# Kernel optimization log

Measured on AMD Instinct MI355X. Metric: run time of the kernel, lower is better.

Reference implementation:

```python
import jax, jax.numpy as jnp
import numpy as np

BIG = 5000.0  # knockout sentinel from the original code
LOSS_WEIGHTS = jnp.array([1.0, 1.0, 1.0, 1.0, 1.0])  # [prob, x, y, a, b]


def _build_targets(preds, targets):
    """Greedy confidence-sorted matching for one batch element.
    preds: [N, 5] (prob, x, y, a, b); targets: [M, 5].
    Returns built targets [N, 5] aligned with the original pred order.
    """
    conf = preds[:, 0]
    order = jnp.argsort(-conf)          # descending confidence
    sp = preds[order]                   # [N, 5] sorted preds
    valid = targets[:, 0] == 1.0        # replaces the torch boolean filter
    n_targs = valid.sum()
    n_pos = (conf > 0.5).sum()
    M = targets.shape[0]

    def step(used, inp):
        i, p = inp
        x, y = p[1], p[2]
        # knocked-out targets sit at (BIG, BIG), matching the in-place write
        tx = jnp.where(used, BIG, targets[:, 1])
        ty = jnp.where(used, BIG, targets[:, 2])
        d2 = (tx - x) ** 2 + (ty - y) ** 2
        d2 = jnp.where(valid, d2, jnp.inf)  # invalid targets were filtered out
        min_idx = jnp.argmin(d2)
        row_nearest = jnp.stack([
            targets[min_idx, 0], tx[min_idx], ty[min_idx],
            targets[min_idx, 3], targets[min_idx, 4],
        ])
        # first valid, not-yet-chosen target (notchosen = x < 5000)
        first_idx = jnp.argmax(valid & (~used))
        row_first = targets[first_idx]
        # false positive: keep pred's continuous vars, prob target = 0
        row_fp = p.at[0].set(0.0)

        case_match = (i < n_pos) & (i < n_targs)   # greedy nearest match + knockout
        case_first = (~case_match) & (i < n_targs)  # n_pos <= i < n_targs
        row = jnp.where(case_match, row_nearest,
                        jnp.where(case_first, row_first, row_fp))
        used = jnp.where(case_match, used.at[min_idx].set(True), used)
        return used, row

    used0 = jnp.zeros(M, dtype=bool)
    _, built = jax.lax.scan(step, used0, (jnp.arange(sp.shape[0]), sp))
    # undo the confidence sort: built_targs[argsort(sort_conf)]
    return built[jnp.argsort(order)]


def setup_inputs() -> dict:
    key = jax.random.key(0)
    k1, k2, k3 = jax.random.split(key, 3)
    B, N, M = 256, 2048, 512
    preds = jax.random.uniform(k1, (B, N, 5), dtype=jnp.float32)  # prob in (0,1) for BCE
    tprob = (jax.random.uniform(k2, (B, M, 1)) > 0.5).astype(jnp.float32)  # ~half valid
    tvals = jax.random.uniform(k3, (B, M, 4), dtype=jnp.float32)
    targets = jnp.concatenate([tprob, tvals], axis=-1)
    return {"preds": preds, "targets": targets}


def reference(preds, targets):
    # built targets are constants w.r.t. autograd (requires_grad=False in torch)
    built = jax.lax.stop_gradient(jax.vmap(_build_targets)(preds, targets))
    p = preds[..., 0]
    t = built[..., 0]
    # BCE with torch's log clamp at -100
    logp = jnp.clip(jnp.log(p), -100.0)
    log1mp = jnp.clip(jnp.log1p(-p), -100.0)
    lossprob = -jnp.mean(t * logp + (1.0 - t) * log1mp) * LOSS_WEIGHTS[0]
    mse = lambda c: jnp.mean((preds[..., c] - built[..., c]) ** 2)
    lossx = mse(1) * LOSS_WEIGHTS[1]
    lossy = mse(2) * LOSS_WEIGHTS[2]
    lossa = mse(3) * LOSS_WEIGHTS[3]
    lossb = mse(4) * LOSS_WEIGHTS[4]
    # dict {'lossx','lossy','lossa','lossb','lossprob'} packed as a 5-vector
    return jnp.stack([lossx, lossy, lossa, lossb, lossprob])
```

## Files before the change

### kernel.cpp

```cpp
#include <hip/hip_runtime.h>
#include <stdint.h>

#define NPRED 2048
#define MT    512
#define BLK   256
#define NCAND 512

template<int C>
__device__ __forceinline__ uint32_t dppminu(uint32_t v) {
  uint32_t o = (uint32_t)__builtin_amdgcn_update_dpp((int)v, (int)v, C, 0xF, 0xF, false);
  return v < o ? v : o;
}
__device__ __forceinline__ uint32_t wave_min_u32_l63(uint32_t v) {
  v = dppminu<0x111>(v); v = dppminu<0x112>(v); v = dppminu<0x114>(v);
  v = dppminu<0x118>(v); v = dppminu<0x142>(v); v = dppminu<0x143>(v);
  return (uint32_t)__builtin_amdgcn_readlane((int)v, 63);
}
__device__ __forceinline__ uint32_t rowmin16(uint32_t v) {
  v = dppminu<0x111>(v); v = dppminu<0x112>(v);
  v = dppminu<0x114>(v); v = dppminu<0x118>(v);
  return v;
}

__global__ __launch_bounds__(BLK, 1) void loss_kernel(const float* __restrict__ preds,
                                                      const float* __restrict__ targets,
                                                      double* __restrict__ acc) {
  const int b = blockIdx.x;
  const float* __restrict__ P = preds   + (size_t)b * NPRED * 5;
  const float* __restrict__ T = targets + (size_t)b * MT * 5;

  __shared__ uint64_t keys[NPRED];
  __shared__ uint64_t cand[NCAND];
  __shared__ float txy[MT * 2];
  __shared__ float tab[MT * 2];
  __shared__ float spx[520], spy[520], spa[520], spb[520];
  __shared__ uint16_t plds[512];
  __shared__ int hist[256];
  __shared__ uint32_t validw[16];
  __shared__ int s_npos, s_nt, s_B, s_ncand, s_first;
  __shared__ uint64_t s_thr;
  __shared__ double red[5][BLK];

  const int tid = threadIdx.x;
  if (tid == 0) { s_npos = 0; s_nt = 0; s_B = 0; s_ncand = 0; s_first = 0; s_thr = 0ull; }
  hist[tid] = 0;
  if (tid < 16) validw[tid] = 0;
  for (int i = tid; i < 520; i += BLK) { spx[i] = 0.f; spy[i] = 0.f; spa[i] = 0.f; spb[i] = 0.f; }
  __syncthreads();

  int cpos = 0;
  for (int i = tid; i < NPRED; i += BLK) {
    float c = P[i * 5 + 0];
    cpos += (c > 0.5f) ? 1 : 0;
    uint32_t cb = __float_as_uint(c);
    keys[i] = ((uint64_t)(~cb) << 32) | (uint32_t)i;
    if (cb >= 0x3F000000u && cb < 0x3F800000u)
      atomicAdd(&hist[(cb >> 15) & 0xFF], 1);
  }
  atomicAdd(&s_npos, cpos);

  int ct = 0;
  for (int m = tid; m < MT; m += BLK) {
    float tp = T[m * 5 + 0];
    bool v = (tp == 1.0f);
    if (v) { ct++; atomicOr(&validw[m >> 5], 1u << (m & 31)); }
    txy[2 * m]     = T[m * 5 + 1];
    txy[2 * m + 1] = T[m * 5 + 2];
    tab[2 * m]     = T[m * 5 + 3];
    tab[2 * m + 1] = T[m * 5 + 4];
  }
  atomicAdd(&s_nt, ct);
  __syncthreads();
  const int n_pos = s_npos;
  const int n_targs = s_nt;

  if (tid < 64) {
    const int lane = tid;
    int4 h4 = *reinterpret_cast<const int4*>(&hist[lane * 4]);
    int t = h4.x + h4.y + h4.z + h4.w;
    int S = t;
#pragma unroll
    for (int off = 1; off < 64; off <<= 1) {
      int o = __shfl_down(S, off);
      if (lane + off < 64) S += o;
    }
    int Snext = S - t;
    int s3 = h4.w + Snext;
    int s2 = h4.z + s3;
    int s1 = h4.y + s2;
    int s0 = h4.x + s1;
    int localB = -1;
    if      (s3 >= n_targs) localB = lane * 4 + 3;
    else if (s2 >= n_targs) localB = lane * 4 + 2;
    else if (s1 >= n_targs) localB = lane * 4 + 1;
    else if (s0 >= n_targs) localB = lane * 4 + 0;
    uint64_t q = __ballot(localB >= 0);
    if (q) {
      int hl = 63 - __clzll((long long)q);
      int B = __builtin_amdgcn_readlane(localB, hl);
      if (lane == 0) s_B = B;
    }
  }
  __syncthreads();
  const int B = s_B;

  for (int i = tid; i < NPRED; i += BLK) {
    uint64_t k = keys[i];
    uint32_t cb = ~(uint32_t)(k >> 32);
    if (cb >= 0x3F000000u && cb < 0x3F800000u && (int)((cb >> 15) & 0xFF) >= B) {
      int slot = atomicAdd(&s_ncand, 1);
      if (slot < NCAND) cand[slot] = k;
    }
  }
  __syncthreads();
  const int ncand = min(s_ncand, NCAND);

  {
    uint64_t ka = (tid < ncand) ? cand[tid] : ~0ull;
    uint64_t kb = (tid + BLK < ncand) ? cand[tid + BLK] : ~0ull;
    int ra = 0, rb = 0;
    for (int j = 0; j < ncand; ++j) {
      uint64_t kj = cand[j];
      ra += (kj < ka) ? 1 : 0;
      rb += (kj < kb) ? 1 : 0;
    }
    if (tid < ncand && ra < n_targs) {
      int idx = (int)(ka & 0xFFFFFFFFu);
      spx[ra] = P[idx * 5 + 1]; spy[ra] = P[idx * 5 + 2];
      spa[ra] = P[idx * 5 + 3]; spb[ra] = P[idx * 5 + 4];
    }
    if (tid < ncand && ra == n_targs - 1) s_thr = ka;
    if (tid + BLK < ncand && rb < n_targs) {
      int idx = (int)(kb & 0xFFFFFFFFu);
      spx[rb] = P[idx * 5 + 1]; spy[rb] = P[idx * 5 + 2];
      spa[rb] = P[idx * 5 + 3]; spb[rb] = P[idx * 5 + 4];
    }
    if (tid + BLK < ncand && rb == n_targs - 1) s_thr = kb;
  }
  __syncthreads();
  const uint64_t thr = s_thr;
  const int K = min(n_pos, n_targs);

  float accp = 0.f;

  if (tid < 64) {
    const int lane = tid;
    const int s = lane & 15;
    const int g = lane >> 4;
    const uint32_t sbase = (uint32_t)(s << 5);

    float txr[32], tyr[32];
#pragma unroll
    for (int j = 0; j < 32; ++j) {
      txr[j] = txy[2 * (s * 32 + j)];
      tyr[j] = txy[2 * (s * 32 + j) + 1];
    }
    uint32_t una = ~validw[s];

    int i = 0;
    float x1 = spx[g], y1 = spy[g];
    float x2 = spx[4 + g], y2 = spy[4 + g];
    while (i + 8 <= K) {
      uint32_t kk1 = 0xFFFFFFFFu, kk2 = 0xFFFFFFFFu;
#pragma unroll
      for (int j = 0; j < 32; ++j) {
        uint32_t pois = 0u - ((una >> j) & 1u);
        {
          float dx = __fsub_rn(txr[j], x1);
          float dy = __fsub_rn(tyr[j], y1);
          float d2 = __fadd_rn(__fmul_rn(dx, dx), __fmul_rn(dy, dy));
          uint32_t key = ((__float_as_uint(d2) & 0xFFFFFE00u) | (sbase + (uint32_t)j)) | pois;
          kk1 = kk1 < key ? kk1 : key;
        }
        {
          float dx = __fsub_rn(txr[j], x2);
          float dy = __fsub_rn(tyr[j], y2);
          float d2 = __fadd_rn(__fmul_rn(dx, dx), __fmul_rn(dy, dy));
          uint32_t key = ((__float_as_uint(d2) & 0xFFFFFE00u) | (sbase + (uint32_t)j)) | pois;
          kk2 = kk2 < key ? kk2 : key;
        }
      }
      kk1 = rowmin16(kk1);
      kk2 = rowmin16(kk2);
      int m0 = __builtin_amdgcn_readlane((int)kk1, 15) & 0x1FF;
      int m1 = __builtin_amdgcn_readlane((int)kk1, 31) & 0x1FF;
      int m2 = __builtin_amdgcn_readlane((int)kk1, 47) & 0x1FF;
      int m3 = __builtin_amdgcn_readlane((int)kk1, 63) & 0x1FF;
      int m4 = __builtin_amdgcn_readlane((int)kk2, 15) & 0x1FF;
      int m5 = __builtin_amdgcn_readlane((int)kk2, 31) & 0x1FF;
      int m6 = __builtin_amdgcn_readlane((int)kk2, 47) & 0x1FF;
      int m7 = __builtin_amdgcn_readlane((int)kk2, 63) & 0x1FF;

      bool c1 = (m1==m0);
      bool c2 = (m2==m0)|(m2==m1);
      bool c3 = (m3==m0)|(m3==m1)|(m3==m2);
      bool c4 = (m4==m0)|(m4==m1)|(m4==m2)|(m4==m3);
      bool c5 = (m5==m0)|(m5==m1)|(m5==m2)|(m5==m3)|(m5==m4);
      bool c6 = (m6==m0)|(m6==m1)|(m6==m2)|(m6==m3)|(m6==m4)|(m6==m5);
      bool c7 = (m7==m0)|(m7==m1)|(m7==m2)|(m7==m3)|(m7==m4)|(m7==m5)|(m7==m6);
      int p = c1 ? 1 : c2 ? 2 : c3 ? 3 : c4 ? 4 : c5 ? 5 : c6 ? 6 : c7 ? 7 : 8;

      int m1e = (p > 1) ? m1 : 0x3FF;
      int m2e = (p > 2) ? m2 : 0x3FF;
      int m3e = (p > 3) ? m3 : 0x3FF;
      int m4e = (p > 4) ? m4 : 0x3FF;
      int m5e = (p > 5) ? m5 : 0x3FF;
      int m6e = (p > 6) ? m6 : 0x3FF;
      int m7e = (p > 7) ? m7 : 0x3FF;

      una |= ((uint32_t)(m0  >> 5) == (uint32_t)s) ? (1u << (m0  & 31)) : 0u;
      una |= ((uint32_t)(m1e >> 5) == (uint32_t)s) ? (1u << (m1e & 31)) : 0u;
      una |= ((uint32_t)(m2e >> 5) == (uint32_t)s) ? (1u << (m2e & 31)) : 0u;
      una |= ((uint32_t)(m3e >> 5) == (uint32_t)s) ? (1u << (m3e & 31)) : 0u;
      una |= ((uint32_t)(m4e >> 5) == (uint32_t)s) ? (1u << (m4e & 31)) : 0u;
      una |= ((uint32_t)(m5e >> 5) == (uint32_t)s) ? (1u << (m5e & 31)) : 0u;
      una |= ((uint32_t)(m6e >> 5) == (uint32_t)s) ? (1u << (m6e & 31)) : 0u;
      una |= ((uint32_t)(m7e >> 5) == (uint32_t)s) ? (1u << (m7e & 31)) : 0u;

      if (lane == 0) {
        plds[i]     = (uint16_t)m0;
        plds[i + 1] = (uint16_t)m1e;
        plds[i + 2] = (uint16_t)m2e;
        plds[i + 3] = (uint16_t)m3e;
        plds[i + 4] = (uint16_t)m4e;
        plds[i + 5] = (uint16_t)m5e;
        plds[i + 6] = (uint16_t)m6e;
        plds[i + 7] = (uint16_t)m7e;
      }
      i += p;
      x1 = spx[i + g];     y1 = spy[i + g];
      x2 = spx[i + 4 + g]; y2 = spy[i + 4 + g];
    }
    while (i < K) {
      float xs = spx[i], ys = spy[i];
      uint32_t kk = 0xFFFFFFFFu;
#pragma unroll
      for (int j = 0; j < 32; ++j) {
        float dx = __fsub_rn(txr[j], xs);
        float dy = __fsub_rn(tyr[j], ys);
        float d2 = __fadd_rn(__fmul_rn(dx, dx), __fmul_rn(dy, dy));
        uint32_t pois = 0u - ((una >> j) & 1u);
        uint32_t key = ((__float_as_uint(d2) & 0xFFFFFE00u) | (sbase + (uint32_t)j)) | pois;
        kk = kk < key ? kk : key;
      }
      kk = rowmin16(kk);
      uint32_t m = (uint32_t)__builtin_amdgcn_readlane((int)kk, 15) & 0x1FFu;
      una |= ((m >> 5) == (uint32_t)s) ? (1u << (m & 31u)) : 0u;
      if (lane == 0) plds[i] = (uint16_t)m;
      ++i;
    }
    uint32_t av = ~una;
    uint32_t fi = av ? (sbase + (uint32_t)__ffs(av) - 1u) : 0xFFFFFFFFu;
    fi = wave_min_u32_l63(fi);
    if (lane == 0) s_first = (fi < MT) ? (int)fi : 0;
  } else {
    for (int i = tid - 64; i < NPRED; i += (BLK - 64)) {
      uint64_t k = keys[i];
      float p = __uint_as_float(~(uint32_t)(k >> 32));
      accp += (k <= thr) ? -fmaxf(logf(p), -100.0f)
                         : -fmaxf(log1pf(-p), -100.0f);
    }
  }
  __syncthreads();

  float ax = 0.f, ay = 0.f, aa = 0.f, ab = 0.f;
  for (int r = tid; r < K; r += BLK) {
    int m = plds[r];
    float dx = __fsub_rn(spx[r], txy[2 * m]);
    float dy = __fsub_rn(spy[r], txy[2 * m + 1]);
    float da = __fsub_rn(spa[r], tab[2 * m]);
    float db = __fsub_rn(spb[r], tab[2 * m + 1]);
    ax += __fmul_rn(dx, dx);
    ay += __fmul_rn(dy, dy);
    aa += __fmul_rn(da, da);
    ab += __fmul_rn(db, db);
  }
  if (n_pos < n_targs) {
    int f = s_first;
    float fx = txy[2 * f], fy = txy[2 * f + 1];
    float fa = tab[2 * f], fb = tab[2 * f + 1];
    for (int i2 = n_pos + tid; i2 < n_targs; i2 += BLK) {
      float dx = __fsub_rn(spx[i2], fx);
      float dy = __fsub_rn(spy[i2], fy);
      float da = __fsub_rn(spa[i2], fa);
      float db = __fsub_rn(spb[i2], fb);
      ax += __fmul_rn(dx, dx);
      ay += __fmul_rn(dy, dy);
      aa += __fmul_rn(da, da);
      ab += __fmul_rn(db, db);
    }
  }

  red[0][tid] = (double)ax;
  red[1][tid] = (double)ay;
  red[2][tid] = (double)aa;
  red[3][tid] = (double)ab;
  red[4][tid] = (double)accp;
  __syncthreads();
  for (int st = BLK / 2; st > 0; st >>= 1) {
    if (tid < st) {
#pragma unroll
      for (int c = 0; c < 5; ++c) red[c][tid] += red[c][tid + st];
    }
    __syncthreads();
  }
  if (tid == 0) {
#pragma unroll
    for (int c = 0; c < 5; ++c) atomicAdd(&acc[c], red[c][0]);
  }
}

__global__ void finalize_kernel(const double* __restrict__ acc,
                                float* __restrict__ out, double inv) {
  int c = threadIdx.x;
  if (c < 5) out[c] = (float)(acc[c] * inv);
}

extern "C" void kernel_launch(void* const* d_in, const int* in_sizes, int n_in,
                              void* d_out, int out_size, void* d_ws, size_t ws_size,
                              hipStream_t stream) {
  const float* preds = (const float*)d_in[0];
  const float* targets = (const float*)d_in[1];
  int B = in_sizes[0] / (NPRED * 5);

  double* acc = (double*)d_ws;
  hipMemsetAsync(acc, 0, 5 * sizeof(double), stream);
  loss_kernel<<<B, BLK, 0, stream>>>(preds, targets, acc);
  finalize_kernel<<<1, 64, 0, stream>>>(acc, (float*)d_out,
                                        1.0 / ((double)B * NPRED));
}
```

Measured before the change: 93.07 us.

## Narrow speculative matching to four preds per wave with split min chains

```diff
diff --git a/kernel.cpp b/kernel.cpp
--- a/kernel.cpp
+++ b/kernel.cpp
@@ -158,93 +158,87 @@
     uint32_t una = ~validw[s];
 
     int i = 0;
-    float x1 = spx[g], y1 = spy[g];
-    float x2 = spx[4 + g], y2 = spy[4 + g];
-    while (i + 8 <= K) {
-      uint32_t kk1 = 0xFFFFFFFFu, kk2 = 0xFFFFFFFFu;
-#pragma unroll
-      for (int j = 0; j < 32; ++j) {
-        uint32_t pois = 0u - ((una >> j) & 1u);
+    float x = spx[g], y = spy[g];
+    while (i + 4 <= K) {
+      float nx1 = spx[i + 1 + g], ny1 = spy[i + 1 + g];
+      float nx2 = spx[i + 2 + g], ny2 = spy[i + 2 + g];
+      float nx3 = spx[i + 3 + g], ny3 = spy[i + 3 + g];
+      float nx4 = spx[i + 4 + g], ny4 = spy[i + 4 + g];
+
+      uint32_t ke = 0xFFFFFFFFu, ko = 0xFFFFFFFFu;
+#pragma unroll
+      for (int j = 0; j < 32; j += 2) {
         {
-          float dx = __fsub_rn(txr[j], x1);
-          float dy = __fsub_rn(tyr[j], y1);
+          float dx = __fsub_rn(txr[j], x);
+          float dy = __fsub_rn(tyr[j], y);
           float d2 = __fadd_rn(__fmul_rn(dx, dx), __fmul_rn(dy, dy));
-          uint32_t key = ((__float_as_uint(d2) & 0xFFFFFE00u) | (sbase + (uint32_t)j)) | pois;
-          kk1 = kk1 < key ? kk1 : key;
+          uint32_t pois = (uint32_t)(((int32_t)(una << (31 - j))) >> 31);
+          uint32_t key = ((__float_as_uint(d2) | pois) & 0xFFFFFE00u) | (uint32_t)j;
+          ke = ke < key ? ke : key;
         }
         {
-          float dx = __fsub_rn(txr[j], x2);
-          float dy = __fsub_rn(tyr[j], y2);
+          float dx = __fsub_rn(txr[j + 1], x);
+          float dy = __fsub_rn(tyr[j + 1], y);
           float d2 = __fadd_rn(__fmul_rn(dx, dx), __fmul_rn(dy, dy));
-          uint32_t key = ((__float_as_uint(d2) & 0xFFFFFE00u) | (sbase + (uint32_t)j)) | pois;
-          kk2 = kk2 < key ? kk2 : key;
+          uint32_t pois = (uint32_t)(((int32_t)(una << (31 - (j + 1)))) >> 31);
+          uint32_t key = ((__float_as_uint(d2) | pois) & 0xFFFFFE00u) | (uint32_t)(j + 1);
+          ko = ko < key ? ko : key;
         }
       }
-      kk1 = rowmin16(kk1);
-      kk2 = rowmin16(kk2);
-      int m0 = __builtin_amdgcn_readlane((int)kk1, 15) & 0x1FF;
-      int m1 = __builtin_amdgcn_readlane((int)kk1, 31) & 0x1FF;
-      int m2 = __builtin_amdgcn_readlane((int)kk1, 47) & 0x1FF;
-      int m3 = __builtin_amdgcn_readlane((int)kk1, 63) & 0x1FF;
-      int m4 = __builtin_amdgcn_readlane((int)kk2, 15) & 0x1FF;
-      int m5 = __builtin_amdgcn_readlane((int)kk2, 31) & 0x1FF;
-      int m6 = __builtin_amdgcn_readlane((int)kk2, 47) & 0x1FF;
-      int m7 = __builtin_amdgcn_readlane((int)kk2, 63) & 0x1FF;
-
-      bool c1 = (m1==m0);
-      bool c2 = (m2==m0)|(m2==m1);
-      bool c3 = (m3==m0)|(m3==m1)|(m3==m2);
-      bool c4 = (m4==m0)|(m4==m1)|(m4==m2)|(m4==m3);
-      bool c5 = (m5==m0)|(m5==m1)|(m5==m2)|(m5==m3)|(m5==m4);
-      bool c6 = (m6==m0)|(m6==m1)|(m6==m2)|(m6==m3)|(m6==m4)|(m6==m5);
-      bool c7 = (m7==m0)|(m7==m1)|(m7==m2)|(m7==m3)|(m7==m4)|(m7==m5)|(m7==m6);
-      int p = c1 ? 1 : c2 ? 2 : c3 ? 3 : c4 ? 4 : c5 ? 5 : c6 ? 6 : c7 ? 7 : 8;
-
+      uint32_t kk = ke < ko ? ke : ko;
+      uint32_t kkg = rowmin16(kk + sbase);
+      int m0 = __builtin_amdgcn_readlane((int)kkg, 15) & 0x1FF;
+      int m1 = __builtin_amdgcn_readlane((int)kkg, 31) & 0x1FF;
+      int m2 = __builtin_amdgcn_readlane((int)kkg, 47) & 0x1FF;
+      int m3 = __builtin_amdgcn_readlane((int)kkg, 63) & 0x1FF;
+
+      int p = (m1 == m0) ? 1
+            : (m2 == m0 || m2 == m1) ? 2
+            : (m3 == m0 || m3 == m1 || m3 == m2) ? 3 : 4;
       int m1e = (p > 1) ? m1 : 0x3FF;
       int m2e = (p > 2) ? m2 : 0x3FF;
       int m3e = (p > 3) ? m3 : 0x3FF;
-      int m4e = (p > 4) ? m4 : 0x3FF;
-      int m5e = (p > 5) ? m5 : 0x3FF;
-      int m6e = (p > 6) ? m6 : 0x3FF;
-      int m7e = (p > 7) ? m7 : 0x3FF;
 
       una |= ((uint32_t)(m0  >> 5) == (uint32_t)s) ? (1u << (m0  & 31)) : 0u;
       una |= ((uint32_t)(m1e >> 5) == (uint32_t)s) ? (1u << (m1e & 31)) : 0u;
       una |= ((uint32_t)(m2e >> 5) == (uint32_t)s) ? (1u << (m2e & 31)) : 0u;
       una |= ((uint32_t)(m3e >> 5) == (uint32_t)s) ? (1u << (m3e & 31)) : 0u;
-      una |= ((uint32_t)(m4e >> 5) == (uint32_t)s) ? (1u << (m4e & 31)) : 0u;
-      una |= ((uint32_t)(m5e >> 5) == (uint32_t)s) ? (1u << (m5e & 31)) : 0u;
-      una |= ((uint32_t)(m6e >> 5) == (uint32_t)s) ? (1u << (m6e & 31)) : 0u;
-      una |= ((uint32_t)(m7e >> 5) == (uint32_t)s) ? (1u << (m7e & 31)) : 0u;
 
       if (lane == 0) {
         plds[i]     = (uint16_t)m0;
         plds[i + 1] = (uint16_t)m1e;
         plds[i + 2] = (uint16_t)m2e;
         plds[i + 3] = (uint16_t)m3e;
-        plds[i + 4] = (uint16_t)m4e;
-        plds[i + 5] = (uint16_t)m5e;
-        plds[i + 6] = (uint16_t)m6e;
-        plds[i + 7] = (uint16_t)m7e;
       }
       i += p;
-      x1 = spx[i + g];     y1 = spy[i + g];
-      x2 = spx[i + 4 + g]; y2 = spy[i + 4 + g];
+      x = (p == 1) ? nx1 : (p == 2) ? nx2 : (p == 3) ? nx3 : nx4;
+      y = (p == 1) ? ny1 : (p == 2) ? ny2 : (p == 3) ? ny3 : ny4;
     }
     while (i < K) {
       float xs = spx[i], ys = spy[i];
-      uint32_t kk = 0xFFFFFFFFu;
-#pragma unroll
-      for (int j = 0; j < 32; ++j) {
-        float dx = __fsub_rn(txr[j], xs);
-        float dy = __fsub_rn(tyr[j], ys);
-        float d2 = __fadd_rn(__fmul_rn(dx, dx), __fmul_rn(dy, dy));
-        uint32_t pois = 0u - ((una >> j) & 1u);
-        uint32_t key = ((__float_as_uint(d2) & 0xFFFFFE00u) | (sbase + (uint32_t)j)) | pois;
-        kk = kk < key ? kk : key;
+      uint32_t ke = 0xFFFFFFFFu, ko = 0xFFFFFFFFu;
+#pragma unroll
+      for (int j = 0; j < 32; j += 2) {
+        {
+          float dx = __fsub_rn(txr[j], xs);
+          float dy = __fsub_rn(tyr[j], ys);
+          float d2 = __fadd_rn(__fmul_rn(dx, dx), __fmul_rn(dy, dy));
+          uint32_t pois = (uint32_t)(((int32_t)(una << (31 - j))) >> 31);
+          uint32_t key = ((__float_as_uint(d2) | pois) & 0xFFFFFE00u) | (uint32_t)j;
+          ke = ke < key ? ke : key;
+        }
+        {
+          float dx = __fsub_rn(txr[j + 1], xs);
+          float dy = __fsub_rn(tyr[j + 1], ys);
+          float d2 = __fadd_rn(__fmul_rn(dx, dx), __fmul_rn(dy, dy));
+          uint32_t pois = (uint32_t)(((int32_t)(una << (31 - (j + 1)))) >> 31);
+          uint32_t key = ((__float_as_uint(d2) | pois) & 0xFFFFFE00u) | (uint32_t)(j + 1);
+          ko = ko < key ? ko : key;
+        }
       }
-      kk = rowmin16(kk);
-      uint32_t m = (uint32_t)__builtin_amdgcn_readlane((int)kk, 15) & 0x1FFu;
+      uint32_t kk = ke < ko ? ke : ko;
+      uint32_t kkg = rowmin16(kk + sbase);
+      uint32_t m = (uint32_t)__builtin_amdgcn_readlane((int)kkg, 15) & 0x1FFu;
       una |= ((m >> 5) == (uint32_t)s) ? (1u << (m & 31u)) : 0u;
       if (lane == 0) plds[i] = (uint16_t)m;
       ++i;
```

Measured after the change: 84.14 us, median of 2. 1.11x faster.
